# Kernel optimization log

Hardware: AMD Instinct MI355X
Metric: run time of the kernel (lower is better)

Reference implementation:

```python
import jax, jax.numpy as jnp
import numpy as np

N_FILTERS = 1024
KH, KW = 5, 5
LOC = 3                      # locality (pad + maxpool kernel/stride)
B, H, W = 1024, 64, 64
WIN = KH + 2 * LOC           # 11: sliced window side after padding


def setup_inputs() -> dict:
    key = jax.random.key(0)
    k1, k2, k3, k4 = jax.random.split(key, 4)
    X = jax.random.normal(k1, (B, 1, H, W), dtype=jnp.float32)
    weight = jax.random.normal(k2, (N_FILTERS, 1, KH, KW), dtype=jnp.float32)
    bias = jax.random.normal(k3, (N_FILTERS,), dtype=jnp.float32)
    # top-left corner (i, j) of each filter's window in the padded image;
    # must satisfy i + KH + 2*LOC <= H + 2*LOC  =>  i in [0, H-KH]
    positions = jax.random.randint(k4, (N_FILTERS, 2), 0, H - KH + 1, dtype=jnp.int32)
    return {"X": X, "weight": weight, "bias": bias, "positions": positions}


def reference(X, weight, bias, positions):
    # ZeroPad2d(locality)
    Xp = jnp.pad(X, ((0, 0), (0, 0), (LOC, LOC), (LOC, LOC)))

    def slice_one(pos):
        return jax.lax.dynamic_slice(Xp, (0, 0, pos[0], pos[1]), (B, 1, WIN, WIN))

    windows = jax.vmap(slice_one)(positions)
    lhs = jnp.transpose(windows[:, :, 0], (1, 0, 2, 3))

    # All n_filters tiny single-channel convs as ONE grouped conv.
    conv = jax.lax.conv_general_dilated(
        lhs, weight, window_strides=(1, 1), padding='VALID',
        dimension_numbers=('NCHW', 'OIHW', 'NCHW'),
        feature_group_count=N_FILTERS)                # [B,F,2L+1,2L+1] = [B,F,7,7]
    conv = conv + bias[None, :, None, None]

    # MaxPool2d((LOC,LOC)) with default stride=LOC, floor mode -> 2x2.
    pooled = jax.lax.reduce_window(
        conv, -jnp.inf, jax.lax.max,
        window_dimensions=(1, 1, LOC, LOC),
        window_strides=(1, 1, LOC, LOC),
        padding='VALID')                              # [B,F,2,2]

    # torch.cat(dim=1) over per-filter [B,1,2,2] tensors + reshape(B,-1)
    return pooled.reshape(B, -1)                      # [B, F*4]
```

## Files before the change

### kernel.cpp

```cpp
#include <hip/hip_runtime.h>

#define N_FILTERS 1024
#define B_TOTAL   1024
#define IMG       64
#define PAD_DIM   70

typedef _Float16 half2_t __attribute__((ext_vector_type(2)));
typedef float    fvec2  __attribute__((ext_vector_type(2)));

__global__ void zero_border_kernel(_Float16* __restrict__ Xt) {
    int pp = blockIdx.x;
    int r = pp / PAD_DIM, c = pp - r * PAD_DIM;
    if (r >= 3 && r < 67 && c >= 3 && c < 67) return;
    unsigned int* q = (unsigned int*)Xt + (size_t)pp * 512;
    q[threadIdx.x] = 0u;
    q[threadIdx.x + 256] = 0u;
}

__global__ __launch_bounds__(256) void transpose_kernel(
    const float* __restrict__ X, _Float16* __restrict__ Xt)
{
    __shared__ float T[64 * 65];
    const int pt = blockIdx.x & 63;
    const int bt = blockIdx.x >> 6;
    const int tx = threadIdx.x & 63, ty = threadIdx.x >> 6;

    #pragma unroll
    for (int pass = 0; pass < 16; ++pass) {
        int bl = pass * 4 + ty;
        T[bl * 65 + tx] = X[(size_t)(bt * 64 + bl) * 4096 + pt * 64 + tx];
    }
    __syncthreads();
    #pragma unroll
    for (int pass = 0; pass < 16; ++pass) {
        int pl = pass * 4 + ty;
        int p  = pt * 64 + pl;
        int r  = p >> 6, c = p & 63;
        Xt[(size_t)((r + 3) * PAD_DIM + (c + 3)) * 1024 + bt * 64 + tx]
            = (_Float16)T[tx * 65 + pl];
    }
}

__global__ __launch_bounds__(256, 3) void filters_main(
    const half2_t* __restrict__ Xt2,
    const float*   __restrict__ W,
    const float*   __restrict__ bias,
    const int*     __restrict__ pos,
    float4*        __restrict__ out4)
{
    const int t    = threadIdx.x;
    const int lane = t & 63;
    const int w    = t >> 6;
    const int bg   = blockIdx.x & 7;
    const int fg   = blockIdx.x >> 3;

    const int f  = fg * 4 + w;
    const int sf = __builtin_amdgcn_readfirstlane(f);
    const int si = __builtin_amdgcn_readfirstlane(pos[2 * sf]);
    const int sj = __builtin_amdgcn_readfirstlane(pos[2 * sf + 1]);

    float wk[25];
    const float* wp = W + sf * 25;
    #pragma unroll
    for (int k = 0; k < 25; ++k) wk[k] = wp[k];

    const int pb = bg * 64 + lane;

    fvec2 acc[36];
    #pragma unroll
    for (int k = 0; k < 36; ++k) acc[k] = (fvec2)0.0f;

    #pragma unroll
    for (int wr = 0; wr < 10; ++wr) {
        const half2_t* rowp = Xt2 + (size_t)((si + wr) * PAD_DIM + sj) * 512 + pb;
        fvec2 in2[10];
        #pragma unroll
        for (int wc = 0; wc < 10; ++wc) {
            half2_t h = rowp[(size_t)wc * 512];
            in2[wc].x = (float)h.x;
            in2[wc].y = (float)h.y;
        }
        #pragma unroll
        for (int y = 0; y < 6; ++y) {
            if (y >= ((wr > 4) ? (wr - 4) : 0) && y <= ((wr < 5) ? wr : 5)) {
                const int r = wr - y;
                #pragma unroll
                for (int x = 0; x < 6; ++x) {
                    #pragma unroll
                    for (int c = 0; c < 5; ++c)
                        acc[y * 6 + x] = wk[r * 5 + c] * in2[x + c] + acc[y * 6 + x];
                }
            }
        }
    }

    const float bv = bias[sf];
    float4 oA, oB;
    {
        float mA[4], mB[4];
        #pragma unroll
        for (int py = 0; py < 2; ++py) {
            #pragma unroll
            for (int px = 0; px < 2; ++px) {
                fvec2 m = acc[(3 * py) * 6 + 3 * px];
                #pragma unroll
                for (int dy = 0; dy < 3; ++dy)
                    #pragma unroll
                    for (int dx = 0; dx < 3; ++dx) {
                        fvec2 v = acc[(3 * py + dy) * 6 + (3 * px + dx)];
                        m.x = fmaxf(m.x, v.x);
                        m.y = fmaxf(m.y, v.y);
                    }
                mA[py * 2 + px] = m.x + bv;
                mB[py * 2 + px] = m.y + bv;
            }
        }
        oA.x = mA[0]; oA.y = mA[1]; oA.z = mA[2]; oA.w = mA[3];
        oB.x = mB[0]; oB.y = mB[1]; oB.z = mB[2]; oB.w = mB[3];
    }

    const int b = bg * 128 + lane * 2;
    out4[(size_t)b * 1024 + f]       = oA;
    out4[(size_t)(b + 1) * 1024 + f] = oB;
}

extern "C" void kernel_launch(void* const* d_in, const int* in_sizes, int n_in,
                              void* d_out, int out_size, void* d_ws, size_t ws_size,
                              hipStream_t stream) {
    const float* X    = (const float*)d_in[0];
    const float* W    = (const float*)d_in[1];
    const float* bias = (const float*)d_in[2];
    const int*   pos  = (const int*)d_in[3];
    float4* out4 = (float4*)d_out;
    _Float16* Xt = (_Float16*)d_ws;

    zero_border_kernel<<<PAD_DIM * PAD_DIM, 256, 0, stream>>>(Xt);
    transpose_kernel<<<1024, 256, 0, stream>>>(X, Xt);
    filters_main<<<2048, 256, 0, stream>>>((const half2_t*)Xt, W, bias, pos, out4);
}
```

Before: 100.2 us.

## Tile transposed image by batch group and stream input pixels into accumulators

```diff
diff --git a/kernel.cpp b/kernel.cpp
--- a/kernel.cpp
+++ b/kernel.cpp
@@ -9,12 +9,23 @@
 typedef float    fvec2  __attribute__((ext_vector_type(2)));
 
 __global__ void zero_border_kernel(_Float16* __restrict__ Xt) {
-    int pp = blockIdx.x;
-    int r = pp / PAD_DIM, c = pp - r * PAD_DIM;
-    if (r >= 3 && r < 67 && c >= 3 && c < 67) return;
-    unsigned int* q = (unsigned int*)Xt + (size_t)pp * 512;
-    q[threadIdx.x] = 0u;
-    q[threadIdx.x + 256] = 0u;
+    int bid = blockIdx.x;
+    int r, c;
+    if (bid < 420) {
+        int r6 = bid / 70;
+        c = bid - r6 * 70;
+        r = (r6 < 3) ? r6 : r6 + 64;
+    } else {
+        int t = bid - 420;
+        r = 3 + t / 6;
+        int k = t - (t / 6) * 6;
+        c = (k < 3) ? k : k + 64;
+    }
+    const size_t pp = (size_t)r * PAD_DIM + c;
+    const int bg = threadIdx.x >> 5, l = threadIdx.x & 31;
+    unsigned long long* q = (unsigned long long*)Xt
+        + (size_t)bg * (4900ull * 32) + pp * 32 + l;
+    *q = 0ull;
 }
 
 __global__ __launch_bounds__(256) void transpose_kernel(
@@ -36,12 +47,12 @@
         int pl = pass * 4 + ty;
         int p  = pt * 64 + pl;
         int r  = p >> 6, c = p & 63;
-        Xt[(size_t)((r + 3) * PAD_DIM + (c + 3)) * 1024 + bt * 64 + tx]
-            = (_Float16)T[tx * 65 + pl];
+        Xt[((size_t)(bt >> 1) * 4900 + (size_t)(r + 3) * PAD_DIM + (c + 3)) * 128
+           + (bt & 1) * 64 + tx] = (_Float16)T[tx * 65 + pl];
     }
 }
 
-__global__ __launch_bounds__(256, 3) void filters_main(
+__global__ __launch_bounds__(256, 4) void filters_main(
     const half2_t* __restrict__ Xt2,
     const float*   __restrict__ W,
     const float*   __restrict__ bias,
@@ -64,7 +75,7 @@
     #pragma unroll
     for (int k = 0; k < 25; ++k) wk[k] = wp[k];
 
-    const int pb = bg * 64 + lane;
+    const half2_t* Xg = Xt2 + (size_t)bg * (4900ull * 64) + lane;
 
     fvec2 acc[36];
     #pragma unroll
@@ -72,23 +83,28 @@
 
     #pragma unroll
     for (int wr = 0; wr < 10; ++wr) {
-        const half2_t* rowp = Xt2 + (size_t)((si + wr) * PAD_DIM + sj) * 512 + pb;
-        fvec2 in2[10];
+        const half2_t* rowp = Xg + (size_t)((si + wr) * PAD_DIM + sj) * 64;
+        const int ylo = (wr > 4) ? (wr - 4) : 0;
+        const int yhi = (wr < 5) ? wr : 5;
         #pragma unroll
         for (int wc = 0; wc < 10; ++wc) {
-            half2_t h = rowp[(size_t)wc * 512];
-            in2[wc].x = (float)h.x;
-            in2[wc].y = (float)h.y;
-        }
-        #pragma unroll
-        for (int y = 0; y < 6; ++y) {
-            if (y >= ((wr > 4) ? (wr - 4) : 0) && y <= ((wr < 5) ? wr : 5)) {
-                const int r = wr - y;
-                #pragma unroll
-                for (int x = 0; x < 6; ++x) {
+            half2_t h = rowp[wc * 64];
+            fvec2 v;
+            v.x = (float)h.x;
+            v.y = (float)h.y;
+            const int xlo = (wc > 4) ? (wc - 4) : 0;
+            const int xhi = (wc < 5) ? wc : 5;
+            #pragma unroll
+            for (int y = 0; y < 6; ++y) {
+                if (y >= ylo && y <= yhi) {
+                    const int r = wr - y;
                     #pragma unroll
-                    for (int c = 0; c < 5; ++c)
-                        acc[y * 6 + x] = wk[r * 5 + c] * in2[x + c] + acc[y * 6 + x];
+                    for (int x = 0; x < 6; ++x) {
+                        if (x >= xlo && x <= xhi) {
+                            const int c = wc - x;
+                            acc[y * 6 + x] = wk[r * 5 + c] * v + acc[y * 6 + x];
+                        }
+                    }
                 }
             }
         }
@@ -134,7 +150,7 @@
     float4* out4 = (float4*)d_out;
     _Float16* Xt = (_Float16*)d_ws;
 
-    zero_border_kernel<<<PAD_DIM * PAD_DIM, 256, 0, stream>>>(Xt);
+    zero_border_kernel<<<804, 256, 0, stream>>>(Xt);
     transpose_kernel<<<1024, 256, 0, stream>>>(X, Xt);
     filters_main<<<2048, 256, 0, stream>>>((const half2_t*)Xt, W, bias, pos, out4);
 }
```

Result: slower. 119.3 us (+19.1%).
